# Optimization experiments

Measured on AMD Instinct MI355X. Metric: run time of the kernel, lower is better.

The kernel has to match this reference:

```python
import jax, jax.numpy as jnp
import numpy as np

B, N, F, E = 256, 784, 1, 6272   # batch, nodes, in-features, edges
C = 32                            # GraphConv channels
H = 512                           # fc1 hidden units
N_OUT = 10


def setup_inputs() -> dict:
    key = jax.random.key(0)
    ks = jax.random.split(key, 12)
    x = jax.random.normal(ks[0], (B, N, F), dtype=jnp.float32)
    edge_row = jax.random.randint(ks[1], (E,), 0, N, dtype=jnp.int32)
    edge_col = jax.random.randint(ks[2], (E,), 0, N, dtype=jnp.int32)
    edge_val = jax.random.uniform(ks[3], (E,), dtype=jnp.float32)
    # GraphConv weights (Glorot-ish scale)
    W1 = jax.random.normal(ks[4], (F, C), dtype=jnp.float32) * 0.5
    b1 = jnp.zeros((C,), dtype=jnp.float32)
    W2 = jax.random.normal(ks[5], (C, C), dtype=jnp.float32) * 0.18
    b2 = jnp.zeros((C,), dtype=jnp.float32)
    # MLP head
    Wf1 = jax.random.normal(ks[6], (N * C, H), dtype=jnp.float32) * 0.01
    bf1 = jnp.zeros((H,), dtype=jnp.float32)
    Wf2 = jax.random.normal(ks[7], (H, N_OUT), dtype=jnp.float32) * 0.04
    bf2 = jnp.zeros((N_OUT,), dtype=jnp.float32)
    return {"x": x, "edge_row": edge_row, "edge_col": edge_col, "edge_val": edge_val,
            "W1": W1, "b1": b1, "W2": W2, "b2": b2,
            "Wf1": Wf1, "bf1": bf1, "Wf2": Wf2, "bf2": bf2}


def _spmm(h, row, col, val):
    # h: [B, N, C]; sparse fltr (COO) @ h per batch element
    msg = jnp.swapaxes(h[:, col, :], 0, 1) * val[:, None, None]      # [E, B, C]
    agg = jax.ops.segment_sum(msg, row, num_segments=N)              # [N, B, C]
    return jnp.swapaxes(agg, 0, 1)                                   # [B, N, C]


def reference(x, edge_row, edge_col, edge_val, W1, b1, W2, b2, Wf1, bf1, Wf2, bf2):
    # GraphConv 1: elu(fltr @ x @ W1 + b1)
    h = jax.nn.elu(_spmm(x, edge_row, edge_col, edge_val) @ W1 + b1)
    # GraphConv 2
    h = jax.nn.elu(_spmm(h, edge_row, edge_col, edge_val) @ W2 + b2)
    # Flatten -> Dense(512, relu) -> Dense(10, softmax)
    flat = h.reshape(B, N * C)
    z = jax.nn.relu(flat @ Wf1 + bf1)
    return jax.nn.softmax(z @ Wf2 + bf2, axis=-1)
```

## Files before the change

kernel.cpp:

```cpp
#include <hip/hip_runtime.h>
#include <hip/hip_bf16.h>

#define B_ 256
#define N_ 784
#define E_ 6272
#define C_ 32
#define H_ 512
#define NK 25088
#define BC 8192
#define S_SPLIT 28

typedef __attribute__((ext_vector_type(8))) short short8;
typedef __attribute__((ext_vector_type(4))) float f32x4;

__device__ __forceinline__ float elu1(float v) {
  return v > 0.f ? v : (__expf(v) - 1.f);
}

__device__ __forceinline__ unsigned short bf16b(float v) {
  __hip_bfloat16 h = __float2bfloat16(v);
  return *reinterpret_cast<unsigned short*>(&h);
}

__device__ __forceinline__ unsigned int pk2(float lo, float hi) {
  return (unsigned int)bf16b(lo) | ((unsigned int)bf16b(hi) << 16);
}

__device__ __forceinline__ void acc2(unsigned u, float val, float& a0, float& a1) {
  float lo = __uint_as_float(u << 16);
  float hi = __uint_as_float(u & 0xffff0000u);
  a0 = fmaf(val, lo, a0);
  a1 = fmaf(val, hi, a1);
}

__global__ __launch_bounds__(1024) void k_prep(
    const int* __restrict__ erow, const int* __restrict__ ecol,
    const float* __restrict__ eval, const float* __restrict__ x,
    const float* __restrict__ Wf1,
    int* __restrict__ row_ptr, int* __restrict__ col_s, float* __restrict__ val_s,
    float* __restrict__ xT, __hip_bfloat16* __restrict__ wf1t) {
  const int t = threadIdx.x;
  if (blockIdx.x == 0) {
    __shared__ int cnt[N_];
    __shared__ int off[N_];
    __shared__ int bufA[1024];
    __shared__ int bufB[1024];
    if (t < N_) cnt[t] = 0;
    __syncthreads();
    for (int e = t; e < E_; e += 1024) atomicAdd(&cnt[erow[e]], 1);
    __syncthreads();
    bufA[t] = (t < N_) ? cnt[t] : 0;
    __syncthreads();
    int* src = bufA; int* dst = bufB;
    for (int d = 1; d < 1024; d <<= 1) {
      int v = src[t];
      if (t >= d) v += src[t - d];
      dst[t] = v;
      __syncthreads();
      int* tmp = src; src = dst; dst = tmp;
    }
    if (t < N_) {
      int ex = src[t] - cnt[t];
      off[t] = ex;
      row_ptr[t] = ex;
    }
    if (t == 0) row_ptr[N_] = E_;
    __syncthreads();
    for (int e = t; e < E_; e += 1024) {
      int r = erow[e];
      int p = atomicAdd(&off[r], 1);
      col_s[p] = ecol[e];
      val_s[p] = eval[e];
    }
  } else if (blockIdx.x <= 200) {
    __shared__ float tile[32][33];
    int bid = blockIdx.x - 1;
    int n0 = (bid % 25) * 32, b0 = (bid / 25) * 32;
    int ni = t & 31, bi = t >> 5;
    int n = n0 + ni;
    if (n < N_) tile[ni][bi] = x[(b0 + bi) * N_ + n];
    __syncthreads();
    int nj = t >> 5, bj = t & 31;
    int nw = n0 + nj;
    if (nw < N_) xT[nw * B_ + b0 + bj] = tile[nj][bj];
  } else {
    __shared__ float tile[64][65];
    int bid = blockIdx.x - 201;
    int k0 = (bid % 392) * 64, n0 = (bid / 392) * 64;
#pragma unroll
    for (int it = 0; it < 4; ++it) {
      int idx = it * 1024 + t;
      int k = idx >> 6, n = idx & 63;
      tile[k][n] = Wf1[(size_t)(k0 + k) * H_ + n0 + n];
    }
    __syncthreads();
#pragma unroll
    for (int it = 0; it < 2; ++it) {
      int idx = it * 1024 + t;
      int n = idx >> 5, kp = idx & 31;
      unsigned int v = pk2(tile[2 * kp][n], tile[2 * kp + 1][n]);
      *reinterpret_cast<unsigned int*>(
          wf1t + (size_t)(n0 + n) * NK + k0 + 2 * kp) = v;
    }
  }
}

__global__ __launch_bounds__(256) void k_gc1(
    const float* __restrict__ xT, const int* __restrict__ row_ptr,
    const int* __restrict__ col_s, const float* __restrict__ val_s,
    const float* __restrict__ W1, const float* __restrict__ b1,
    __hip_bfloat16* __restrict__ h1) {
  __shared__ int lc[64];
  __shared__ float lv[64];
  int n = blockIdx.x, t = threadIdx.x;
  int e0 = row_ptr[n], deg = row_ptr[n + 1] - e0;
  float agg = 0.f;
  for (int base = 0; base < deg; base += 64) {
    int m = min(64, deg - base);
    __syncthreads();
    if (t < m) { lc[t] = col_s[e0 + base + t]; lv[t] = val_s[e0 + base + t]; }
    __syncthreads();
    int e = 0;
    for (; e + 4 <= m; e += 4) {
      float x0 = xT[lc[e + 0] * B_ + t];
      float x1 = xT[lc[e + 1] * B_ + t];
      float x2 = xT[lc[e + 2] * B_ + t];
      float x3 = xT[lc[e + 3] * B_ + t];
      agg = fmaf(lv[e + 0], x0, agg);
      agg = fmaf(lv[e + 1], x1, agg);
      agg = fmaf(lv[e + 2], x2, agg);
      agg = fmaf(lv[e + 3], x3, agg);
    }
    for (; e < m; ++e)
      agg = fmaf(lv[e], xT[lc[e] * B_ + t], agg);
  }
  union { unsigned int u[16]; uint4 v[4]; } ob;
#pragma unroll
  for (int c = 0; c < C_; c += 2) {
    float o0 = elu1(fmaf(agg, W1[c], b1[c]));
    float o1 = elu1(fmaf(agg, W1[c + 1], b1[c + 1]));
    ob.u[c >> 1] = pk2(o0, o1);
  }
  uint4* dst = reinterpret_cast<uint4*>(h1 + (size_t)n * BC + t * C_);
#pragma unroll
  for (int j = 0; j < 4; ++j) dst[j] = ob.v[j];
}

__global__ __launch_bounds__(64) void k_gc2(
    const __hip_bfloat16* __restrict__ h1, const int* __restrict__ row_ptr,
    const int* __restrict__ col_s, const float* __restrict__ val_s,
    const float* __restrict__ W2, const float* __restrict__ b2,
    __hip_bfloat16* __restrict__ flat) {
  __shared__ int lc[64];
  __shared__ float lv[64];
  int bid = blockIdx.x;
  int q = bid & 3;
  int n = bid >> 2;
  int t = threadIdx.x;
  int tb = q * 64 + t;
  int e0 = row_ptr[n], deg = row_ptr[n + 1] - e0;
  float acc[C_];
#pragma unroll
  for (int c = 0; c < C_; ++c) acc[c] = 0.f;

#define ACC16(v0, v1, v2, v3, val) do {                                       \
    acc2(v0.x, val, acc[0], acc[1]);  acc2(v0.y, val, acc[2], acc[3]);        \
    acc2(v0.z, val, acc[4], acc[5]);  acc2(v0.w, val, acc[6], acc[7]);        \
    acc2(v1.x, val, acc[8], acc[9]);  acc2(v1.y, val, acc[10], acc[11]);      \
    acc2(v1.z, val, acc[12], acc[13]); acc2(v1.w, val, acc[14], acc[15]);     \
    acc2(v2.x, val, acc[16], acc[17]); acc2(v2.y, val, acc[18], acc[19]);     \
    acc2(v2.z, val, acc[20], acc[21]); acc2(v2.w, val, acc[22], acc[23]);     \
    acc2(v3.x, val, acc[24], acc[25]); acc2(v3.y, val, acc[26], acc[27]);     \
    acc2(v3.z, val, acc[28], acc[29]); acc2(v3.w, val, acc[30], acc[31]);     \
  } while (0)

  for (int base = 0; base < deg; base += 64) {
    int m = min(64, deg - base);
    __syncthreads();
    if (t < m) { lc[t] = col_s[e0 + base + t]; lv[t] = val_s[e0 + base + t]; }
    __syncthreads();
    int e = 0;
    for (; e + 4 <= m; e += 4) {
      const uint4* p0 = reinterpret_cast<const uint4*>(h1 + (size_t)lc[e + 0] * BC + tb * C_);
      const uint4* p1 = reinterpret_cast<const uint4*>(h1 + (size_t)lc[e + 1] * BC + tb * C_);
      const uint4* p2 = reinterpret_cast<const uint4*>(h1 + (size_t)lc[e + 2] * BC + tb * C_);
      const uint4* p3 = reinterpret_cast<const uint4*>(h1 + (size_t)lc[e + 3] * BC + tb * C_);
      uint4 a0 = p0[0], a1 = p0[1], a2 = p0[2], a3 = p0[3];
      uint4 b0 = p1[0], b1 = p1[1], b2v = p1[2], b3 = p1[3];
      uint4 c0 = p2[0], c1 = p2[1], c2 = p2[2], c3 = p2[3];
      uint4 d0 = p3[0], d1 = p3[1], d2 = p3[2], d3 = p3[3];
      float va = lv[e], vb = lv[e + 1], vc = lv[e + 2], vd = lv[e + 3];
      ACC16(a0, a1, a2, a3, va);
      ACC16(b0, b1, b2v, b3, vb);
      ACC16(c0, c1, c2, c3, vc);
      ACC16(d0, d1, d2, d3, vd);
    }
    for (; e < m; ++e) {
      const uint4* p0 = reinterpret_cast<const uint4*>(h1 + (size_t)lc[e] * BC + tb * C_);
      uint4 a0 = p0[0], a1 = p0[1], a2 = p0[2], a3 = p0[3];
      ACC16(a0, a1, a2, a3, lv[e]);
    }
  }
#undef ACC16

  union { unsigned int u[16]; uint4 v[4]; } ob;
#pragma unroll
  for (int c2 = 0; c2 < C_; c2 += 2) {
    float o0 = b2[c2], o1 = b2[c2 + 1];
#pragma unroll
    for (int c = 0; c < C_; ++c) {
      o0 = fmaf(acc[c], W2[c * C_ + c2], o0);
      o1 = fmaf(acc[c], W2[c * C_ + c2 + 1], o1);
    }
    ob.u[c2 >> 1] = pk2(elu1(o0), elu1(o1));
  }
  uint4* dst = reinterpret_cast<uint4*>(flat + (size_t)tb * NK + n * C_);
#pragma unroll
  for (int j = 0; j < 4; ++j) dst[j] = ob.v[j];
}

__global__ __launch_bounds__(256, 2) void k_fc1(
    const __hip_bfloat16* __restrict__ flat, const __hip_bfloat16* __restrict__ wf1t,
    float* __restrict__ partial) {
  __shared__ unsigned char lds[3 * 24576];
  int raw = blockIdx.x;
  int bid = (raw & 7) * 56 + (raw >> 3);
  int s = bid >> 4, r16 = bid & 15;
  int m0 = (r16 & 1) * 128;
  int n0 = (r16 >> 1) * 64;
  int k0 = s * 896;
  int tid = threadIdx.x;
  int w = tid >> 6, l = tid & 63;
  int r = l & 15, g = l >> 4;

  const __hip_bfloat16* src[6];
  int ldsoff[6];
#pragma unroll
  for (int j = 0; j < 6; ++j) {
    int reg = w * 6 + j;
    ldsoff[j] = reg * 1024 + l * 16;
    if (reg < 16) {
      int fmg = reg >> 1, ks = reg & 1;
      src[j] = flat + (size_t)(m0 + fmg * 16 + r) * NK + (k0 + ks * 32 + g * 8);
    } else {
      int fng = (reg - 16) >> 1, ks = reg & 1;
      src[j] = wf1t + (size_t)(n0 + fng * 16 + r) * NK + (k0 + ks * 32 + g * 8);
    }
  }

  f32x4 acc[4][2];
#pragma unroll
  for (int i = 0; i < 4; ++i)
#pragma unroll
    for (int j = 0; j < 2; ++j) acc[i][j] = (f32x4){0.f, 0.f, 0.f, 0.f};

#define GLOAD_LDS(gp, lp)                                                     \
  __builtin_amdgcn_global_load_lds(                                           \
      (const __attribute__((address_space(1))) unsigned int*)(gp),            \
      (__attribute__((address_space(3))) unsigned int*)(lp), 16, 0, 0)
#define STAGE(t, buf) do {                                                    \
    _Pragma("unroll")                                                         \
    for (int j = 0; j < 6; ++j)                                               \
      GLOAD_LDS(src[j] + (t) * 64, &lds[(buf) * 24576 + ldsoff[j]]);          \
  } while (0)
#define VWAIT(n) do {                                                         \
    asm volatile("s_waitcnt vmcnt(%0)" :: "n"(n) : "memory");                 \
    __builtin_amdgcn_sched_barrier(0);                                        \
  } while (0)
#define BAR() do {                                                            \
    __builtin_amdgcn_s_barrier();                                             \
    __builtin_amdgcn_sched_barrier(0);                                        \
  } while (0)
#define COMPUTE(buf) do {                                                     \
    const unsigned char* bb = &lds[(buf) * 24576];                            \
    short8 af[4][2], bf[2][2];                                                \
    _Pragma("unroll")                                                         \
    for (int fm = 0; fm < 4; ++fm)                                            \
      _Pragma("unroll")                                                       \
      for (int ks = 0; ks < 2; ++ks)                                          \
        af[fm][ks] = *reinterpret_cast<const short8*>(                        \
            bb + (((4 * (w & 1) + fm) * 2 + ks) << 10) + l * 16);             \
    _Pragma("unroll")                                                         \
    for (int fn = 0; fn < 2; ++fn)                                            \
      _Pragma("unroll")                                                       \
      for (int ks = 0; ks < 2; ++ks)                                          \
        bf[fn][ks] = *reinterpret_cast<const short8*>(                        \
            bb + ((16 + (2 * (w >> 1) + fn) * 2 + ks) << 10) + l * 16);       \
    _Pragma("unroll")                                                         \
    for (int ks = 0; ks < 2; ++ks)                                            \
      _Pragma("unroll")                                                       \
      for (int fn = 0; fn < 2; ++fn)                                          \
        _Pragma("unroll")                                                     \
        for (int fm = 0; fm < 4; ++fm)                                        \
          acc[fm][fn] = __builtin_amdgcn_mfma_f32_16x16x32_bf16(              \
              af[fm][ks], bf[fn][ks], acc[fm][fn], 0, 0, 0);                  \
  } while (0)
#define STEP(t) do {                                                          \
    VWAIT((t) < 13 ? 6 : 0);                                                  \
    BAR();                                                                    \
    if ((t) + 2 <= 13) STAGE((t) + 2, ((t) + 2) % 3);                         \
    COMPUTE((t) % 3);                                                         \
  } while (0)

  STAGE(0, 0);
  STAGE(1, 1);
  STEP(0);  STEP(1);  STEP(2);  STEP(3);  STEP(4);  STEP(5);  STEP(6);
  STEP(7);  STEP(8);  STEP(9);  STEP(10); STEP(11); STEP(12); STEP(13);

#undef GLOAD_LDS
#undef STAGE
#undef VWAIT
#undef BAR
#undef COMPUTE
#undef STEP

  int wm = (w & 1) * 64, wn = (w >> 1) * 32;
  float* p = partial + (size_t)s * (256 * 512);
#pragma unroll
  for (int fm = 0; fm < 4; ++fm)
#pragma unroll
    for (int fn = 0; fn < 2; ++fn)
#pragma unroll
      for (int q = 0; q < 4; ++q) {
        int m = m0 + wm + fm * 16 + g * 4 + q;
        int n = n0 + wn + fn * 16 + r;
        p[m * 512 + n] = acc[fm][fn][q];
      }
}

__global__ __launch_bounds__(512) void k_head(
    const float* __restrict__ partial, const float* __restrict__ bf1,
    const float* __restrict__ Wf2, const float* __restrict__ bf2,
    float* __restrict__ out) {
  __shared__ float red[8][12];
  int b = blockIdx.x;
  int t = threadIdx.x;
  float v = bf1[t];
#pragma unroll
  for (int s = 0; s < S_SPLIT; ++s)
    v += partial[(size_t)s * (256 * 512) + b * 512 + t];
  v = fmaxf(v, 0.f);
  float pacc[10];
#pragma unroll
  for (int j = 0; j < 10; ++j) pacc[j] = v * Wf2[t * 10 + j];
#pragma unroll
  for (int j = 0; j < 10; ++j)
#pragma unroll
    for (int d = 32; d > 0; d >>= 1)
      pacc[j] += __shfl_down(pacc[j], d);
  int wv = t >> 6, ln = t & 63;
  if (ln == 0) {
#pragma unroll
    for (int j = 0; j < 10; ++j) red[wv][j] = pacc[j];
  }
  __syncthreads();
  if (t == 0) {
    float lg[10];
    float m = -1e30f;
#pragma unroll
    for (int j = 0; j < 10; ++j) {
      float z = bf2[j];
#pragma unroll
      for (int wq = 0; wq < 8; ++wq) z += red[wq][j];
      lg[j] = z;
      m = fmaxf(m, z);
    }
    float sum = 0.f;
#pragma unroll
    for (int j = 0; j < 10; ++j) { lg[j] = __expf(lg[j] - m); sum += lg[j]; }
    float inv = 1.f / sum;
#pragma unroll
    for (int j = 0; j < 10; ++j) out[b * 10 + j] = lg[j] * inv;
  }
}

extern "C" void kernel_launch(void* const* d_in, const int* in_sizes, int n_in,
                              void* d_out, int out_size, void* d_ws, size_t ws_size,
                              hipStream_t stream) {
  const float* x    = (const float*)d_in[0];
  const int*   erow = (const int*)d_in[1];
  const int*   ecol = (const int*)d_in[2];
  const float* ev   = (const float*)d_in[3];
  const float* W1   = (const float*)d_in[4];
  const float* b1   = (const float*)d_in[5];
  const float* W2   = (const float*)d_in[6];
  const float* b2   = (const float*)d_in[7];
  const float* Wf1  = (const float*)d_in[8];
  const float* bf1  = (const float*)d_in[9];
  const float* Wf2  = (const float*)d_in[10];
  const float* bf2  = (const float*)d_in[11];
  float* out = (float*)d_out;

  const size_t partial_bytes = (size_t)S_SPLIT * 256 * 512 * 4;
  const size_t flat_bytes    = (size_t)B_ * NK * 2;
  const size_t wf1t_bytes    = (size_t)H_ * NK * 2;

  char* ws = (char*)d_ws;
  float* partial = (float*)ws;
  float* xT = (float*)ws;
  __hip_bfloat16* h1 = (__hip_bfloat16*)(ws + 802816);
  __hip_bfloat16* flat = (__hip_bfloat16*)(ws + partial_bytes);
  __hip_bfloat16* wf1t = (__hip_bfloat16*)(ws + partial_bytes + flat_bytes);
  char* tail = ws + partial_bytes + flat_bytes + wf1t_bytes;
  int*   row_ptr = (int*)tail;
  int*   col_s   = (int*)(tail + 3152);
  float* val_s   = (float*)(tail + 3152 + E_ * 4);

  hipLaunchKernelGGL(k_prep, dim3(1 + 200 + 392 * 8), dim3(1024), 0, stream,
                     erow, ecol, ev, x, Wf1, row_ptr, col_s, val_s, xT, wf1t);
  hipLaunchKernelGGL(k_gc1, dim3(N_), dim3(256), 0, stream,
                     xT, row_ptr, col_s, val_s, W1, b1, h1);
  hipLaunchKernelGGL(k_gc2, dim3(N_ * 4), dim3(64), 0, stream,
                     h1, row_ptr, col_s, val_s, W2, b2, flat);
  hipLaunchKernelGGL(k_fc1, dim3(S_SPLIT * 16), dim3(256), 0, stream,
                     flat, wf1t, partial);
  hipLaunchKernelGGL(k_head, dim3(B_), dim3(512), 0, stream,
                     partial, bf1, Wf2, bf2, out);
}
```

Measured before the change: 92.32 us.

## Split Wf1 bf16 transpose across the two GraphConv kernels to overlap with gathers

Removes the Wf1 fp32-to-bf16 transpose from the prep kernel. The first half of K is converted by extra blocks appended to the gc1 launch, and the second half by extra blocks appended to the gc2 launch. The aim is to let this bandwidth-heavy conversion run alongside the latency-bound sparse gather kernels instead of as its own phase. Shared memory is unioned with the gather buffers, which enlarges LDS per gc1 block and may reduce occupancy for the graph-conv blocks.

```diff
diff --git a/kernel.cpp b/kernel.cpp
--- a/kernel.cpp
+++ b/kernel.cpp
@@ -9,6 +9,7 @@
 #define NK 25088
 #define BC 8192
 #define S_SPLIT 28
+#define KHALF 12544
 
 typedef __attribute__((ext_vector_type(8))) short short8;
 typedef __attribute__((ext_vector_type(4))) float f32x4;
@@ -36,9 +37,8 @@
 __global__ __launch_bounds__(1024) void k_prep(
     const int* __restrict__ erow, const int* __restrict__ ecol,
     const float* __restrict__ eval, const float* __restrict__ x,
-    const float* __restrict__ Wf1,
     int* __restrict__ row_ptr, int* __restrict__ col_s, float* __restrict__ val_s,
-    float* __restrict__ xT, __hip_bfloat16* __restrict__ wf1t) {
+    float* __restrict__ xT) {
   const int t = threadIdx.x;
   if (blockIdx.x == 0) {
     __shared__ int cnt[N_];
@@ -72,7 +72,7 @@
       col_s[p] = ecol[e];
       val_s[p] = eval[e];
     }
-  } else if (blockIdx.x <= 200) {
+  } else {
     __shared__ float tile[32][33];
     int bid = blockIdx.x - 1;
     int n0 = (bid % 25) * 32, b0 = (bid / 25) * 32;
@@ -83,25 +83,6 @@
     int nj = t >> 5, bj = t & 31;
     int nw = n0 + nj;
     if (nw < N_) xT[nw * B_ + b0 + bj] = tile[nj][bj];
-  } else {
-    __shared__ float tile[64][65];
-    int bid = blockIdx.x - 201;
-    int k0 = (bid % 392) * 64, n0 = (bid / 392) * 64;
-#pragma unroll
-    for (int it = 0; it < 4; ++it) {
-      int idx = it * 1024 + t;
-      int k = idx >> 6, n = idx & 63;
-      tile[k][n] = Wf1[(size_t)(k0 + k) * H_ + n0 + n];
-    }
-    __syncthreads();
-#pragma unroll
-    for (int it = 0; it < 2; ++it) {
-      int idx = it * 1024 + t;
-      int n = idx >> 5, kp = idx & 31;
-      unsigned int v = pk2(tile[2 * kp][n], tile[2 * kp + 1][n]);
-      *reinterpret_cast<unsigned int*>(
-          wf1t + (size_t)(n0 + n) * NK + k0 + 2 * kp) = v;
-    }
   }
 }
 
@@ -109,59 +90,87 @@
     const float* __restrict__ xT, const int* __restrict__ row_ptr,
     const int* __restrict__ col_s, const float* __restrict__ val_s,
     const float* __restrict__ W1, const float* __restrict__ b1,
+    const float* __restrict__ Wf1, __hip_bfloat16* __restrict__ wf1t,
     __hip_bfloat16* __restrict__ h1) {
-  __shared__ int lc[64];
-  __shared__ float lv[64];
-  int n = blockIdx.x, t = threadIdx.x;
-  int e0 = row_ptr[n], deg = row_ptr[n + 1] - e0;
-  float agg = 0.f;
-  for (int base = 0; base < deg; base += 64) {
-    int m = min(64, deg - base);
-    __syncthreads();
-    if (t < m) { lc[t] = col_s[e0 + base + t]; lv[t] = val_s[e0 + base + t]; }
-    __syncthreads();
-    int e = 0;
-    for (; e + 4 <= m; e += 4) {
-      float x0 = xT[lc[e + 0] * B_ + t];
-      float x1 = xT[lc[e + 1] * B_ + t];
-      float x2 = xT[lc[e + 2] * B_ + t];
-      float x3 = xT[lc[e + 3] * B_ + t];
-      agg = fmaf(lv[e + 0], x0, agg);
-      agg = fmaf(lv[e + 1], x1, agg);
-      agg = fmaf(lv[e + 2], x2, agg);
-      agg = fmaf(lv[e + 3], x3, agg);
-    }
-    for (; e < m; ++e)
-      agg = fmaf(lv[e], xT[lc[e] * B_ + t], agg);
-  }
-  union { unsigned int u[16]; uint4 v[4]; } ob;
-#pragma unroll
-  for (int c = 0; c < C_; c += 2) {
-    float o0 = elu1(fmaf(agg, W1[c], b1[c]));
-    float o1 = elu1(fmaf(agg, W1[c + 1], b1[c + 1]));
-    ob.u[c >> 1] = pk2(o0, o1);
-  }
-  uint4* dst = reinterpret_cast<uint4*>(h1 + (size_t)n * BC + t * C_);
-#pragma unroll
-  for (int j = 0; j < 4; ++j) dst[j] = ob.v[j];
+  __shared__ union {
+    struct { int lc[64]; float lv[64]; } g;
+    float tile[64][65];
+  } sm;
+  int t = threadIdx.x;
+  if (blockIdx.x < N_) {
+    int n = blockIdx.x;
+    int e0 = row_ptr[n], deg = row_ptr[n + 1] - e0;
+    float agg = 0.f;
+    for (int base = 0; base < deg; base += 64) {
+      int m = min(64, deg - base);
+      __syncthreads();
+      if (t < m) { sm.g.lc[t] = col_s[e0 + base + t]; sm.g.lv[t] = val_s[e0 + base + t]; }
+      __syncthreads();
+      int e = 0;
+      for (; e + 4 <= m; e += 4) {
+        float x0 = xT[sm.g.lc[e + 0] * B_ + t];
+        float x1 = xT[sm.g.lc[e + 1] * B_ + t];
+        float x2 = xT[sm.g.lc[e + 2] * B_ + t];
+        float x3 = xT[sm.g.lc[e + 3] * B_ + t];
+        agg = fmaf(sm.g.lv[e + 0], x0, agg);
+        agg = fmaf(sm.g.lv[e + 1], x1, agg);
+        agg = fmaf(sm.g.lv[e + 2], x2, agg);
+        agg = fmaf(sm.g.lv[e + 3], x3, agg);
+      }
+      for (; e < m; ++e)
+        agg = fmaf(sm.g.lv[e], xT[sm.g.lc[e] * B_ + t], agg);
+    }
+    union { unsigned int u[16]; uint4 v[4]; } ob;
+#pragma unroll
+    for (int c = 0; c < C_; c += 2) {
+      float o0 = elu1(fmaf(agg, W1[c], b1[c]));
+      float o1 = elu1(fmaf(agg, W1[c + 1], b1[c + 1]));
+      ob.u[c >> 1] = pk2(o0, o1);
+    }
+    uint4* dst = reinterpret_cast<uint4*>(h1 + (size_t)n * BC + t * C_);
+#pragma unroll
+    for (int j = 0; j < 4; ++j) dst[j] = ob.v[j];
+  } else {
+    int bid = blockIdx.x - N_;
+    int k0 = (bid % 196) * 64, n0 = (bid / 196) * 64;
+#pragma unroll
+    for (int it = 0; it < 16; ++it) {
+      int idx = it * 256 + t;
+      int kk = idx >> 6, nn = idx & 63;
+      sm.tile[kk][nn] = Wf1[(size_t)(k0 + kk) * H_ + n0 + nn];
+    }
+    __syncthreads();
+#pragma unroll
+    for (int it = 0; it < 8; ++it) {
+      int idx = it * 256 + t;
+      int nn = idx >> 5, kp = idx & 31;
+      unsigned int v = pk2(sm.tile[2 * kp][nn], sm.tile[2 * kp + 1][nn]);
+      *reinterpret_cast<unsigned int*>(
+          wf1t + (size_t)(n0 + nn) * NK + k0 + 2 * kp) = v;
+    }
+  }
 }
 
 __global__ __launch_bounds__(64) void k_gc2(
     const __hip_bfloat16* __restrict__ h1, const int* __restrict__ row_ptr,
     const int* __restrict__ col_s, const float* __restrict__ val_s,
     const float* __restrict__ W2, const float* __restrict__ b2,
+    const float* __restrict__ Wf1, __hip_bfloat16* __restrict__ wf1t,
     __hip_bfloat16* __restrict__ flat) {
-  __shared__ int lc[64];
-  __shared__ float lv[64];
+  __shared__ union {
+    struct { int lc[64]; float lv[64]; } g;
+    float tile[32][33];
+  } sm;
   int bid = blockIdx.x;
-  int q = bid & 3;
-  int n = bid >> 2;
   int t = threadIdx.x;
-  int tb = q * 64 + t;
-  int e0 = row_ptr[n], deg = row_ptr[n + 1] - e0;
-  float acc[C_];
-#pragma unroll
-  for (int c = 0; c < C_; ++c) acc[c] = 0.f;
+  if (bid < N_ * 4) {
+    int q = bid & 3;
+    int n = bid >> 2;
+    int tb = q * 64 + t;
+    int e0 = row_ptr[n], deg = row_ptr[n + 1] - e0;
+    float acc[C_];
+#pragma unroll
+    for (int c = 0; c < C_; ++c) acc[c] = 0.f;
 
 #define ACC16(v0, v1, v2, v3, val) do {                                       \
     acc2(v0.x, val, acc[0], acc[1]);  acc2(v0.y, val, acc[2], acc[3]);        \
@@ -174,49 +183,68 @@
     acc2(v3.z, val, acc[28], acc[29]); acc2(v3.w, val, acc[30], acc[31]);     \
   } while (0)
 
-  for (int base = 0; base < deg; base += 64) {
-    int m = min(64, deg - base);
-    __syncthreads();
-    if (t < m) { lc[t] = col_s[e0 + base + t]; lv[t] = val_s[e0 + base + t]; }
-    __syncthreads();
-    int e = 0;
-    for (; e + 4 <= m; e += 4) {
-      const uint4* p0 = reinterpret_cast<const uint4*>(h1 + (size_t)lc[e + 0] * BC + tb * C_);
-      const uint4* p1 = reinterpret_cast<const uint4*>(h1 + (size_t)lc[e + 1] * BC + tb * C_);
-      const uint4* p2 = reinterpret_cast<const uint4*>(h1 + (size_t)lc[e + 2] * BC + tb * C_);
-      const uint4* p3 = reinterpret_cast<const uint4*>(h1 + (size_t)lc[e + 3] * BC + tb * C_);
-      uint4 a0 = p0[0], a1 = p0[1], a2 = p0[2], a3 = p0[3];
-      uint4 b0 = p1[0], b1 = p1[1], b2v = p1[2], b3 = p1[3];
-      uint4 c0 = p2[0], c1 = p2[1], c2 = p2[2], c3 = p2[3];
-      uint4 d0 = p3[0], d1 = p3[1], d2 = p3[2], d3 = p3[3];
-      float va = lv[e], vb = lv[e + 1], vc = lv[e + 2], vd = lv[e + 3];
-      ACC16(a0, a1, a2, a3, va);
-      ACC16(b0, b1, b2v, b3, vb);
-      ACC16(c0, c1, c2, c3, vc);
-      ACC16(d0, d1, d2, d3, vd);
-    }
-    for (; e < m; ++e) {
-      const uint4* p0 = reinterpret_cast<const uint4*>(h1 + (size_t)lc[e] * BC + tb * C_);
-      uint4 a0 = p0[0], a1 = p0[1], a2 = p0[2], a3 = p0[3];
-      ACC16(a0, a1, a2, a3, lv[e]);
-    }
-  }
+    for (int base = 0; base < deg; base += 64) {
+      int m = min(64, deg - base);
+      __syncthreads();
+      if (t < m) { sm.g.lc[t] = col_s[e0 + base + t]; sm.g.lv[t] = val_s[e0 + base + t]; }
+      __syncthreads();
+      int e = 0;
+      for (; e + 4 <= m; e += 4) {
+        const uint4* p0 = reinterpret_cast<const uint4*>(h1 + (size_t)sm.g.lc[e + 0] * BC + tb * C_);
+        const uint4* p1 = reinterpret_cast<const uint4*>(h1 + (size_t)sm.g.lc[e + 1] * BC + tb * C_);
+        const uint4* p2 = reinterpret_cast<const uint4*>(h1 + (size_t)sm.g.lc[e + 2] * BC + tb * C_);
+        const uint4* p3 = reinterpret_cast<const uint4*>(h1 + (size_t)sm.g.lc[e + 3] * BC + tb * C_);
+        uint4 a0 = p0[0], a1 = p0[1], a2 = p0[2], a3 = p0[3];
+        uint4 b0 = p1[0], b1 = p1[1], b2v = p1[2], b3 = p1[3];
+        uint4 c0 = p2[0], c1 = p2[1], c2 = p2[2], c3 = p2[3];
+        uint4 d0 = p3[0], d1 = p3[1], d2 = p3[2], d3 = p3[3];
+        float va = sm.g.lv[e], vb = sm.g.lv[e + 1], vc = sm.g.lv[e + 2], vd = sm.g.lv[e + 3];
+        ACC16(a0, a1, a2, a3, va);
+        ACC16(b0, b1, b2v, b3, vb);
+        ACC16(c0, c1, c2, c3, vc);
+        ACC16(d0, d1, d2, d3, vd);
+      }
+      for (; e < m; ++e) {
+        const uint4* p0 = reinterpret_cast<const uint4*>(h1 + (size_t)sm.g.lc[e] * BC + tb * C_);
+        uint4 a0 = p0[0], a1 = p0[1], a2 = p0[2], a3 = p0[3];
+        ACC16(a0, a1, a2, a3, sm.g.lv[e]);
+      }
+    }
 #undef ACC16
 
-  union { unsigned int u[16]; uint4 v[4]; } ob;
-#pragma unroll
-  for (int c2 = 0; c2 < C_; c2 += 2) {
-    float o0 = b2[c2], o1 = b2[c2 + 1];
-#pragma unroll
-    for (int c = 0; c < C_; ++c) {
-      o0 = fmaf(acc[c], W2[c * C_ + c2], o0);
-      o1 = fmaf(acc[c], W2[c * C_ + c2 + 1], o1);
-    }
-    ob.u[c2 >> 1] = pk2(elu1(o0), elu1(o1));
-  }
-  uint4* dst = reinterpret_cast<uint4*>(flat + (size_t)tb * NK + n * C_);
-#pragma unroll
-  for (int j = 0; j < 4; ++j) dst[j] = ob.v[j];
+    union { unsigned int u[16]; uint4 v[4]; } ob;
+#pragma unroll
+    for (int c2 = 0; c2 < C_; c2 += 2) {
+      float o0 = b2[c2], o1 = b2[c2 + 1];
+#pragma unroll
+      for (int c = 0; c < C_; ++c) {
+        o0 = fmaf(acc[c], W2[c * C_ + c2], o0);
+        o1 = fmaf(acc[c], W2[c * C_ + c2 + 1], o1);
+      }
+      ob.u[c2 >> 1] = pk2(elu1(o0), elu1(o1));
+    }
+    uint4* dst = reinterpret_cast<uint4*>(flat + (size_t)tb * NK + n * C_);
+#pragma unroll
+    for (int j = 0; j < 4; ++j) dst[j] = ob.v[j];
+  } else {
+    int bid2 = bid - N_ * 4;
+    int k0 = KHALF + (bid2 % 392) * 32, n0 = (bid2 / 392) * 32;
+#pragma unroll
+    for (int it = 0; it < 16; ++it) {
+      int idx = it * 64 + t;
+      int kk = idx >> 5, nn = idx & 31;
+      sm.tile[kk][nn] = Wf1[(size_t)(k0 + kk) * H_ + n0 + nn];
+    }
+    __syncthreads();
+#pragma unroll
+    for (int it = 0; it < 8; ++it) {
+      int idx = it * 64 + t;
+      int nn = idx >> 4, kp = idx & 15;
+      unsigned int v = pk2(sm.tile[2 * kp][nn], sm.tile[2 * kp + 1][nn]);
+      *reinterpret_cast<unsigned int*>(
+          wf1t + (size_t)(n0 + nn) * NK + k0 + 2 * kp) = v;
+    }
+  }
 }
 
 __global__ __launch_bounds__(256, 2) void k_fc1(
@@ -406,12 +434,12 @@
   int*   col_s   = (int*)(tail + 3152);
   float* val_s   = (float*)(tail + 3152 + E_ * 4);
 
-  hipLaunchKernelGGL(k_prep, dim3(1 + 200 + 392 * 8), dim3(1024), 0, stream,
-                     erow, ecol, ev, x, Wf1, row_ptr, col_s, val_s, xT, wf1t);
-  hipLaunchKernelGGL(k_gc1, dim3(N_), dim3(256), 0, stream,
-                     xT, row_ptr, col_s, val_s, W1, b1, h1);
-  hipLaunchKernelGGL(k_gc2, dim3(N_ * 4), dim3(64), 0, stream,
-                     h1, row_ptr, col_s, val_s, W2, b2, flat);
+  hipLaunchKernelGGL(k_prep, dim3(1 + 200), dim3(1024), 0, stream,
+                     erow, ecol, ev, x, row_ptr, col_s, val_s, xT);
+  hipLaunchKernelGGL(k_gc1, dim3(N_ + 196 * 8), dim3(256), 0, stream,
+                     xT, row_ptr, col_s, val_s, W1, b1, Wf1, wf1t, h1);
+  hipLaunchKernelGGL(k_gc2, dim3(N_ * 4 + 392 * 16), dim3(64), 0, stream,
+                     h1, row_ptr, col_s, val_s, W2, b2, Wf1, wf1t, flat);
   hipLaunchKernelGGL(k_fc1, dim3(S_SPLIT * 16), dim3(256), 0, stream,
                      flat, wf1t, partial);
   hipLaunchKernelGGL(k_head, dim3(B_), dim3(512), 0, stream,
```

Result: faster. 90.28 us (-2.2%).
